# Performance work log

Measured on AMD Instinct MI355X. Metric: run time of the kernel, lower is better.

Reference implementation:

```python
import jax, jax.numpy as jnp
import numpy as np

EPS = 1e-15
B, N, F, K = 16, 1024, 512, 128  # graphs, max_nodes, feat dim, clusters


def setup_inputs() -> dict:
    key = jax.random.key(0)
    k0, k1, k2 = jax.random.split(key, 3)
    rng = np.random.default_rng(0)
    # Ragged graph sizes (between N/2 and N nodes per graph)
    counts = rng.integers(N // 2, N + 1, size=B)
    T = int(counts.sum())
    batch = np.repeat(np.arange(B), counts)
    starts = np.repeat(np.concatenate([[0], np.cumsum(counts)[:-1]]), counts)
    column = np.arange(T) - starts
    flat_index = batch * N + column  # as in _build_motifpool_dense_layout
    mask_flat = np.zeros(B * N, dtype=bool)
    mask_flat[flat_index] = True
    mask = mask_flat.reshape(B, N)
    x = jax.random.normal(k0, (T, F), dtype=jnp.float32)
    s = jax.random.normal(k1, (T, K), dtype=jnp.float32)
    a = jax.random.uniform(k2, (B, N, N), dtype=jnp.float32)
    m = jnp.asarray(mask)
    adj = (a + a.transpose(0, 2, 1)) * m[:, :, None] * m[:, None, :]
    return {
        'x': x,
        's': s,
        'adj': adj,
        'flat_index': jnp.asarray(flat_index, dtype=jnp.int32),
        'mask': m,
    }


def reference(x, s, adj, flat_index, mask):
    Bn, Nn = mask.shape
    Fd = x.shape[-1]
    Kd = s.shape[-1]
    # ragged -> dense scatter (index_copy_ equivalent)
    xd = jnp.zeros((Bn * Nn, Fd), x.dtype).at[flat_index].set(x).reshape(Bn, Nn, Fd)
    sd = jnp.zeros((Bn * Nn, Kd), s.dtype).at[flat_index].set(s).reshape(Bn, Nn, Kd)
    fmask = mask[..., None].astype(x.dtype)  # [B,N,1]
    sm = jax.nn.softmax(sd, axis=-1) * fmask
    xm = xd * fmask
    # pooled features and adjacency
    out = jnp.einsum('bnk,bnf->bkf', sm, xm)
    sa = jnp.einsum('bnk,bnm->bkm', sm, adj)
    out_adj = jnp.einsum('bkm,bml->bkl', sa, sm)
    # mincut loss: tr(S^T A S) / tr(S^T D S)
    mincut_num = jnp.trace(out_adj, axis1=-2, axis2=-1)
    d_flat = adj.sum(-1)  # node degrees [B,N]
    mincut_den = jnp.einsum('bn,bnk,bnk->b', d_flat, sm, sm)
    mincut_loss = jnp.mean(-(mincut_num / mincut_den))
    # orthogonality loss
    ss = jnp.einsum('bnk,bnl->bkl', sm, sm)
    ss_norm = jnp.linalg.norm(ss, axis=(-2, -1), keepdims=True)
    i_s = jnp.eye(Kd, dtype=ss.dtype)
    ortho_loss = jnp.mean(
        jnp.linalg.norm(ss / ss_norm - i_s / jnp.sqrt(jnp.asarray(Kd, ss.dtype)),
                        axis=(-2, -1)))
    # zero diagonal, symmetric degree-normalize
    eye_b = jnp.eye(Kd, dtype=bool)
    out_adj = jnp.where(eye_b, jnp.zeros((), out_adj.dtype), out_adj)
    d = jnp.sqrt(out_adj.sum(-1))[:, None, :] + EPS  # [B,1,K]
    out_adj = out_adj / d / d.transpose(0, 2, 1)
    return (sm, out, out_adj, mincut_loss, ortho_loss)
```

## Files before the change

kernel.cpp:

```cpp
#include <hip/hip_runtime.h>

constexpr int NB = 16, NN = 1024, NF = 512, NK = 128;
constexpr int NCH = 8;
constexpr int MSPLIT = 2;
constexpr float EPSV = 1e-15f;

__global__ __launch_bounds__(256) void k_build_rowof(const int* __restrict__ fidx,
                                                     int* __restrict__ rowof, int T) {
  int t = blockIdx.x * 256 + threadIdx.x;
  if (t < T) rowof[fidx[t]] = t;
}

__global__ __launch_bounds__(256) void k_softmax(const float* __restrict__ s,
                                                 const int* __restrict__ rowof,
                                                 float* __restrict__ sm) {
  int d = blockIdx.x * 4 + (threadIdx.x >> 6);
  int lane = threadIdx.x & 63;
  float* orow = sm + (size_t)d * NK;
  int ri = rowof[d];
  if (ri < 0) {
    orow[lane] = 0.f;
    orow[lane + 64] = 0.f;
    return;
  }
  const float* row = s + (size_t)ri * NK;
  float a = row[lane], b2 = row[lane + 64];
  float m = fmaxf(a, b2);
#pragma unroll
  for (int off = 32; off; off >>= 1) m = fmaxf(m, __shfl_xor(m, off, 64));
  float e0 = expf(a - m), e1 = expf(b2 - m);
  float ssum = e0 + e1;
#pragma unroll
  for (int off = 32; off; off >>= 1) ssum += __shfl_xor(ssum, off, 64);
  float inv = 1.0f / ssum;
  orow[lane] = e0 * inv;
  orow[lane + 64] = e1 * inv;
}

__global__ __launch_bounds__(256) void k_adj_sm(const float* __restrict__ adj,
                                                const float* __restrict__ sm,
                                                float* __restrict__ Yp,
                                                float* __restrict__ dfp) {
  __shared__ float At[64][68];
  __shared__ float Ss[64][128];
  int b = blockIdx.y;
  int n0 = blockIdx.x * 64;
  int z = blockIdx.z;
  const float* A = adj + (size_t)b * NN * NN;
  const float* S = sm + (size_t)b * NN * NK;
  int tid = threadIdx.x;
  int tr = tid >> 4, tc = tid & 15;
  int r0 = tr * 4, c0 = tc * 8;
  float acc[4][8] = {};
  float rsum[4] = {0.f, 0.f, 0.f, 0.f};
  for (int m0 = z * (NN / MSPLIT); m0 < (z + 1) * (NN / MSPLIT); m0 += 64) {
    __syncthreads();
#pragma unroll
    for (int p = 0; p < 4; ++p) {
      int r = p * 16 + tr;
      float4 v = *(const float4*)(A + (size_t)(n0 + r) * NN + m0 + tc * 4);
      *(float4*)&At[r][tc * 4] = v;
      float ps = v.x + v.y + v.z + v.w;
      ps += __shfl_xor(ps, 1, 64); ps += __shfl_xor(ps, 2, 64);
      ps += __shfl_xor(ps, 4, 64); ps += __shfl_xor(ps, 8, 64);
      rsum[p] += ps;
    }
#pragma unroll
    for (int p = 0; p < 8; ++p) {
      int r = p * 8 + (tid >> 5);
      int c = (tid & 31) * 4;
      *(float4*)&Ss[r][c] = *(const float4*)(S + (size_t)(m0 + r) * NK + c);
    }
    __syncthreads();
#pragma unroll
    for (int mm = 0; mm < 64; ++mm) {
      float a0 = At[r0 + 0][mm], a1 = At[r0 + 1][mm];
      float a2 = At[r0 + 2][mm], a3 = At[r0 + 3][mm];
      float bb[8];
      *(float4*)&bb[0] = *(const float4*)&Ss[mm][c0];
      *(float4*)&bb[4] = *(const float4*)&Ss[mm][c0 + 4];
#pragma unroll
      for (int j = 0; j < 8; ++j) {
        acc[0][j] = fmaf(a0, bb[j], acc[0][j]);
        acc[1][j] = fmaf(a1, bb[j], acc[1][j]);
        acc[2][j] = fmaf(a2, bb[j], acc[2][j]);
        acc[3][j] = fmaf(a3, bb[j], acc[3][j]);
      }
    }
  }
  float* Yb = Yp + ((size_t)z * NB + b) * NN * NK;
#pragma unroll
  for (int i = 0; i < 4; ++i) {
    *(float4*)(Yb + (size_t)(n0 + r0 + i) * NK + c0) = *(float4*)&acc[i][0];
    *(float4*)(Yb + (size_t)(n0 + r0 + i) * NK + c0 + 4) = *(float4*)&acc[i][4];
  }
  if (tc == 0) {
#pragma unroll
    for (int p = 0; p < 4; ++p)
      dfp[((size_t)z * NB + b) * NN + n0 + p * 16 + tr] = rsum[p];
  }
}

__global__ __launch_bounds__(256) void k_dflat(const float* __restrict__ dfp,
                                               float* __restrict__ dflat) {
  int i = blockIdx.x * 256 + threadIdx.x;
  dflat[i] = dfp[i] + dfp[NB * NN + i];
}

__global__ __launch_bounds__(512) void k_feat(const float* __restrict__ sm,
                                              const float* __restrict__ x,
                                              const int* __restrict__ rowof,
                                              float* __restrict__ out0,
                                              float* __restrict__ out1) {
  __shared__ float Ss[64][128];
  __shared__ float Xs[64][68];
  int b = blockIdx.y;
  int fbase = blockIdx.x * 64;
  int z = blockIdx.z;
  const float* S = sm + (size_t)b * NN * NK;
  int tid = threadIdx.x;
  int tk = tid >> 4, tf = tid & 15;
  int k0 = tk * 4, f0 = tf * 4;
  float acc[4][4] = {};
  for (int n0 = z * (NN / 2); n0 < (z + 1) * (NN / 2); n0 += 64) {
    __syncthreads();
#pragma unroll
    for (int p = 0; p < 4; ++p) {
      int r = p * 16 + (tid >> 5);
      int c = (tid & 31) * 4;
      *(float4*)&Ss[r][c] = *(const float4*)(S + (size_t)(n0 + r) * NK + c);
    }
#pragma unroll
    for (int p = 0; p < 2; ++p) {
      int r = p * 32 + (tid >> 4);
      int c = (tid & 15) * 4;
      int ri = rowof[b * NN + n0 + r];
      float4 v = make_float4(0.f, 0.f, 0.f, 0.f);
      if (ri >= 0) v = *(const float4*)(x + (size_t)ri * NF + fbase + c);
      *(float4*)&Xs[r][c] = v;
    }
    __syncthreads();
#pragma unroll
    for (int nn = 0; nn < 64; ++nn) {
      float a[4], bb[4];
      *(float4*)a = *(const float4*)&Ss[nn][k0];
      *(float4*)bb = *(const float4*)&Xs[nn][f0];
#pragma unroll
      for (int i = 0; i < 4; ++i)
#pragma unroll
        for (int j = 0; j < 4; ++j)
          acc[i][j] = fmaf(a[i], bb[j], acc[i][j]);
    }
  }
  float* O = (z ? out1 : out0) + (size_t)b * NK * NF;
#pragma unroll
  for (int i = 0; i < 4; ++i)
    *(float4*)(O + (size_t)(k0 + i) * NF + fbase + f0) = *(float4*)&acc[i][0];
}

__global__ __launch_bounds__(256) void k_red_feat(float* __restrict__ out0,
                                                  const float* __restrict__ out1) {
  size_t i = (size_t)blockIdx.x * 256 + threadIdx.x;
  float4 a = ((const float4*)out0)[i];
  float4 c = ((const float4*)out1)[i];
  a.x += c.x; a.y += c.y; a.z += c.z; a.w += c.w;
  ((float4*)out0)[i] = a;
}

__global__ __launch_bounds__(512) void k_tt(const float* __restrict__ sm,
                                            const float* __restrict__ Yp,
                                            const float* __restrict__ dflat,
                                            float* __restrict__ padj,
                                            float* __restrict__ pss,
                                            float* __restrict__ denb) {
  __shared__ float Ls[32][128];
  __shared__ float Rs[32][128];
  __shared__ float red[512];
  int ch = blockIdx.x, b = blockIdx.y, z = blockIdx.z;
  int nbase = ch * 128;
  const float* L = sm + (size_t)b * NN * NK;
  const float* R0 = Yp + (size_t)b * NN * NK;
  const float* R1 = Yp + ((size_t)NB + b) * NN * NK;
  float* O = (z ? pss : padj) + ((size_t)ch * NB + b) * NK * NK;
  int tid = threadIdx.x;
  int tkk = tid >> 5, tcc = tid & 31;
  int k0 = tkk * 8, c0 = tcc * 4;
  int lr = tid >> 4, c4 = tid & 15;
  float acc[8][4] = {};
  float denp = 0.f;
  float (&RR)[32][128] = z ? Ls : Rs;
  for (int n0 = 0; n0 < 128; n0 += 32) {
    __syncthreads();
    int grow = nbase + n0 + lr;
    const float* Lp = L + (size_t)grow * NK;
    float df = z ? dflat[b * NN + grow] : 0.f;
#pragma unroll
    for (int j = 0; j < 2; ++j) {
      int cc = (c4 + 16 * j) * 4;
      float4 v = *(const float4*)(Lp + cc);
      *(float4*)&Ls[lr][cc] = v;
      if (z) {
        denp += df * (v.x * v.x + v.y * v.y + v.z * v.z + v.w * v.w);
      } else {
        float4 r0v = *(const float4*)(R0 + (size_t)grow * NK + cc);
        float4 r1v = *(const float4*)(R1 + (size_t)grow * NK + cc);
        r0v.x += r1v.x; r0v.y += r1v.y; r0v.z += r1v.z; r0v.w += r1v.w;
        *(float4*)&Rs[lr][cc] = r0v;
      }
    }
    __syncthreads();
#pragma unroll
    for (int nn = 0; nn < 32; ++nn) {
      float a[8], bb[4];
      *(float4*)&a[0] = *(const float4*)&Ls[nn][k0];
      *(float4*)&a[4] = *(const float4*)&Ls[nn][k0 + 4];
      *(float4*)bb = *(const float4*)&RR[nn][c0];
#pragma unroll
      for (int i = 0; i < 8; ++i)
#pragma unroll
        for (int j = 0; j < 4; ++j)
          acc[i][j] = fmaf(a[i], bb[j], acc[i][j]);
    }
  }
#pragma unroll
  for (int i = 0; i < 8; ++i)
    *(float4*)&O[(size_t)(k0 + i) * NK + c0] = *(float4*)&acc[i][0];
  if (z) {
    red[tid] = denp;
    __syncthreads();
#pragma unroll
    for (int sft = 256; sft; sft >>= 1) {
      if (tid < sft) red[tid] += red[tid + sft];
      __syncthreads();
    }
    if (tid == 0) atomicAdd(&denb[b], red[0]);
  }
}

__global__ __launch_bounds__(256) void k_reduce(const float* __restrict__ padj,
                                                const float* __restrict__ pss,
                                                float* __restrict__ adjraw,
                                                float* __restrict__ ssb) {
  size_t i = (size_t)blockIdx.x * 256 + threadIdx.x;
  size_t stride4 = (size_t)NB * NK * NK / 4;
  const float4* pa = (const float4*)padj + i;
  const float4* ps = (const float4*)pss + i;
  float4 a = make_float4(0.f, 0.f, 0.f, 0.f);
  float4 s = make_float4(0.f, 0.f, 0.f, 0.f);
#pragma unroll
  for (int ch = 0; ch < NCH; ++ch) {
    float4 va = pa[(size_t)ch * stride4];
    float4 vs = ps[(size_t)ch * stride4];
    a.x += va.x; a.y += va.y; a.z += va.z; a.w += va.w;
    s.x += vs.x; s.y += vs.y; s.z += vs.z; s.w += vs.w;
  }
  ((float4*)adjraw)[i] = a;
  ((float4*)ssb)[i] = s;
}

__device__ __forceinline__ float block_reduce_sum(float v, float* red) {
  int tid = threadIdx.x;
  red[tid] = v;
  __syncthreads();
#pragma unroll
  for (int sft = 128; sft; sft >>= 1) {
    if (tid < sft) red[tid] += red[tid + sft];
    __syncthreads();
  }
  float r = red[0];
  __syncthreads();
  return r;
}

__global__ __launch_bounds__(256) void k_finalize(const float* __restrict__ denb,
                                                  const float* __restrict__ ssb,
                                                  float* __restrict__ out_adj,
                                                  float* __restrict__ out_loss) {
  __shared__ float red[256];
  __shared__ float sd[NK];
  int b = blockIdx.x, tid = threadIdx.x;
  float* AR = out_adj + (size_t)b * NK * NK;
  const float* SS = ssb + (size_t)b * NK * NK;

  float tv = (tid < NK) ? AR[tid * NK + tid] : 0.f;
  float trace = block_reduce_sum(tv, red);
  float den = denb[b];

  float n2 = 0.f;
  for (int i4 = tid; i4 < NK * NK / 4; i4 += 256) {
    float4 v = *(const float4*)(SS + (size_t)i4 * 4);
    n2 += v.x * v.x + v.y * v.y + v.z * v.z + v.w * v.w;
  }
  float nrm = sqrtf(block_reduce_sum(n2, red));

  const float isk = 0.08838834764831845f;
  float osum = 0.f;
  for (int i = tid; i < NK * NK; i += 256) {
    int r = i >> 7, c = i & (NK - 1);
    float val = SS[i] / nrm - ((r == c) ? isk : 0.f);
    osum += val * val;
  }
  float ortho = sqrtf(block_reduce_sum(osum, red));

  if (tid < NK) {
    float rsumv = 0.f;
    const float* row = AR + (size_t)tid * NK;
    for (int j = 0; j < NK; ++j) rsumv += (j == tid) ? 0.f : row[j];
    sd[tid] = sqrtf(rsumv) + EPSV;
  }
  __syncthreads();

  for (int i = tid; i < NK * NK; i += 256) {
    int r = i >> 7, c = i & (NK - 1);
    AR[i] = (r == c) ? 0.f : AR[i] / (sd[r] * sd[c]);
  }

  if (tid == 0) {
    atomicAdd(&out_loss[0], -(trace / den) * (1.0f / NB));
    atomicAdd(&out_loss[1], ortho * (1.0f / NB));
  }
}

extern "C" void kernel_launch(void* const* d_in, const int* in_sizes, int n_in,
                              void* d_out, int out_size, void* d_ws, size_t ws_size,
                              hipStream_t stream) {
  const float* x = (const float*)d_in[0];
  const float* s = (const float*)d_in[1];
  const float* adj = (const float*)d_in[2];
  const int* fidx = (const int*)d_in[3];
  int T = in_sizes[3];

  float* out_sm = (float*)d_out;
  float* out_feat = out_sm + (size_t)NB * NN * NK;
  float* out_adj = out_feat + (size_t)NB * NK * NF;
  float* out_loss = out_adj + (size_t)NB * NK * NK;

  float* Yp = (float*)d_ws;
  float* dfp = Yp + (size_t)MSPLIT * NB * NN * NK;
  float* dflat = dfp + (size_t)MSPLIT * NB * NN;
  float* padj = dflat + (size_t)NB * NN;
  float* pss = padj + (size_t)NCH * NB * NK * NK;
  float* ssb = pss + (size_t)NCH * NB * NK * NK;
  float* outf1 = ssb + (size_t)NB * NK * NK;
  float* denb = outf1 + (size_t)NB * NK * NF;
  int* rowof = (int*)(denb + NB);

  hipMemsetAsync(out_loss, 0, 2 * sizeof(float), stream);
  hipMemsetAsync(denb, 0, NB * sizeof(float), stream);
  hipMemsetAsync(rowof, 0xFF, (size_t)NB * NN * sizeof(int), stream);

  k_build_rowof<<<(T + 255) / 256, 256, 0, stream>>>(fidx, rowof, T);
  k_softmax<<<NB * NN / 4, 256, 0, stream>>>(s, rowof, out_sm);
  k_adj_sm<<<dim3(NN / 64, NB, MSPLIT), 256, 0, stream>>>(adj, out_sm, Yp, dfp);
  k_dflat<<<NB * NN / 256, 256, 0, stream>>>(dfp, dflat);
  k_feat<<<dim3(NF / 64, NB, 2), 512, 0, stream>>>(out_sm, x, rowof, out_feat, outf1);
  k_red_feat<<<NB * NK * NF / 4 / 256, 256, 0, stream>>>(out_feat, outf1);
  k_tt<<<dim3(NCH, NB, 2), 512, 0, stream>>>(out_sm, Yp, dflat, padj, pss, denb);
  k_reduce<<<NB * NK * NK / 4 / 256, 256, 0, stream>>>(padj, pss, out_adj, ssb);
  k_finalize<<<NB, 256, 0, stream>>>(denb, ssb, out_adj, out_loss);
}
```

Before: 285.2 us.

## Use split-bf16 MFMA for adjacency and pooled-product GEMMs with transposed softmax

Moves the adj×S and S^T×Y / S^T×S products from scalar FP32 FMA loops onto bf16 MFMA instructions. Operands are split into hi and lo bf16 parts and combined with three MFMAs per tile so accuracy stays close to FP32. The softmax kernel now also writes a transposed hi/lo bf16 copy of S, and Y is stored transposed so both GEMMs get K-contiguous operands. The aim is to cut the ALU-bound FP32 matmul time, at the cost of extra workspace traffic, more conversion work, and small precision loss from the three-term split.

```diff
diff --git a/kernel.cpp b/kernel.cpp
--- a/kernel.cpp
+++ b/kernel.cpp
@@ -5,6 +5,26 @@
 constexpr int MSPLIT = 2;
 constexpr float EPSV = 1e-15f;
 
+typedef __attribute__((ext_vector_type(8))) short bf16x8;
+typedef __attribute__((ext_vector_type(4))) float f32x4;
+
+__device__ __forceinline__ f32x4 MFMA(bf16x8 a, bf16x8 b, f32x4 c) {
+  return __builtin_amdgcn_mfma_f32_16x16x32_bf16(a, b, c, 0, 0, 0);
+}
+
+__device__ __forceinline__ unsigned short bf16_rn(float f) {
+  unsigned int u = __float_as_uint(f);
+  u += 0x7fffu + ((u >> 16) & 1u);
+  return (unsigned short)(u >> 16);
+}
+__device__ __forceinline__ float bf16f(unsigned short h) {
+  return __uint_as_float((unsigned int)h << 16);
+}
+__device__ __forceinline__ void split2(float f, unsigned short& h, unsigned short& lo) {
+  h = bf16_rn(f);
+  lo = bf16_rn(f - bf16f(h));
+}
+
 __global__ __launch_bounds__(256) void k_build_rowof(const int* __restrict__ fidx,
                                                      int* __restrict__ rowof, int T) {
   int t = blockIdx.x * 256 + threadIdx.x;
@@ -13,92 +33,137 @@
 
 __global__ __launch_bounds__(256) void k_softmax(const float* __restrict__ s,
                                                  const int* __restrict__ rowof,
-                                                 float* __restrict__ sm) {
-  int d = blockIdx.x * 4 + (threadIdx.x >> 6);
-  int lane = threadIdx.x & 63;
-  float* orow = sm + (size_t)d * NK;
-  int ri = rowof[d];
-  if (ri < 0) {
-    orow[lane] = 0.f;
-    orow[lane + 64] = 0.f;
-    return;
-  }
-  const float* row = s + (size_t)ri * NK;
-  float a = row[lane], b2 = row[lane + 64];
-  float m = fmaxf(a, b2);
-#pragma unroll
-  for (int off = 32; off; off >>= 1) m = fmaxf(m, __shfl_xor(m, off, 64));
-  float e0 = expf(a - m), e1 = expf(b2 - m);
-  float ssum = e0 + e1;
-#pragma unroll
-  for (int off = 32; off; off >>= 1) ssum += __shfl_xor(ssum, off, 64);
-  float inv = 1.0f / ssum;
-  orow[lane] = e0 * inv;
-  orow[lane + 64] = e1 * inv;
+                                                 float* __restrict__ sm,
+                                                 unsigned short* __restrict__ smTh,
+                                                 unsigned short* __restrict__ smTl) {
+  __shared__ float P[64][129];
+  int blk = blockIdx.x;
+  int b = blk >> 4, n0 = (blk & 15) * 64;
+  int tid = threadIdx.x, wv = tid >> 6, lane = tid & 63;
+  for (int i = 0; i < 16; ++i) {
+    int r = wv * 16 + i;
+    int ri = rowof[b * NN + n0 + r];
+    float e0 = 0.f, e1 = 0.f;
+    if (ri >= 0) {
+      const float* row = s + (size_t)ri * NK;
+      float a = row[lane], c = row[lane + 64];
+      float m = fmaxf(a, c);
+#pragma unroll
+      for (int off = 32; off; off >>= 1) m = fmaxf(m, __shfl_xor(m, off, 64));
+      e0 = expf(a - m);
+      e1 = expf(c - m);
+      float sum = e0 + e1;
+#pragma unroll
+      for (int off = 32; off; off >>= 1) sum += __shfl_xor(sum, off, 64);
+      float inv = 1.0f / sum;
+      e0 *= inv;
+      e1 *= inv;
+    }
+    P[r][lane] = e0;
+    P[r][lane + 64] = e1;
+  }
+  __syncthreads();
+  int r2 = tid >> 2, cb = (tid & 3) * 32;
+  float* orow = sm + ((size_t)b * NN + n0 + r2) * NK + cb;
+#pragma unroll
+  for (int j = 0; j < 8; ++j) {
+    float4 v = make_float4(P[r2][cb + j * 4], P[r2][cb + j * 4 + 1],
+                           P[r2][cb + j * 4 + 2], P[r2][cb + j * 4 + 3]);
+    *(float4*)(orow + j * 4) = v;
+  }
+  for (int j = 0; j < 32; ++j) {
+    int k = wv * 32 + j;
+    float v = P[lane][k];
+    unsigned short h, lo;
+    split2(v, h, lo);
+    size_t off = ((size_t)b * NK + k) * NN + n0 + lane;
+    smTh[off] = h;
+    smTl[off] = lo;
+  }
 }
 
 __global__ __launch_bounds__(256) void k_adj_sm(const float* __restrict__ adj,
-                                                const float* __restrict__ sm,
-                                                float* __restrict__ Yp,
+                                                const unsigned short* __restrict__ smTh,
+                                                const unsigned short* __restrict__ smTl,
+                                                float* __restrict__ Ytp,
                                                 float* __restrict__ dfp) {
-  __shared__ float At[64][68];
-  __shared__ float Ss[64][128];
-  int b = blockIdx.y;
-  int n0 = blockIdx.x * 64;
-  int z = blockIdx.z;
+  __shared__ __align__(16) unsigned short STh[128][72], STl[128][72];
+  __shared__ __align__(16) unsigned short ADh[64][72], ADl[64][72];
+  int b = blockIdx.y, n0 = blockIdx.x * 64, z = blockIdx.z;
+  int tid = threadIdx.x, wv = tid >> 6, l = tid & 63;
+  int lr = l & 15, lk = l >> 4;
+  int tk = tid >> 1, th = tid & 1;
+  int sn = tid >> 2, sq = tid & 3;
   const float* A = adj + (size_t)b * NN * NN;
-  const float* S = sm + (size_t)b * NN * NK;
-  int tid = threadIdx.x;
-  int tr = tid >> 4, tc = tid & 15;
-  int r0 = tr * 4, c0 = tc * 8;
-  float acc[4][8] = {};
-  float rsum[4] = {0.f, 0.f, 0.f, 0.f};
+  f32x4 zero = {0.f, 0.f, 0.f, 0.f};
+  f32x4 acc[2][4];
+#pragma unroll
+  for (int i = 0; i < 2; ++i)
+#pragma unroll
+    for (int j = 0; j < 4; ++j) acc[i][j] = zero;
+  float rsacc = 0.f;
   for (int m0 = z * (NN / MSPLIT); m0 < (z + 1) * (NN / MSPLIT); m0 += 64) {
     __syncthreads();
-#pragma unroll
-    for (int p = 0; p < 4; ++p) {
-      int r = p * 16 + tr;
-      float4 v = *(const float4*)(A + (size_t)(n0 + r) * NN + m0 + tc * 4);
-      *(float4*)&At[r][tc * 4] = v;
-      float ps = v.x + v.y + v.z + v.w;
-      ps += __shfl_xor(ps, 1, 64); ps += __shfl_xor(ps, 2, 64);
-      ps += __shfl_xor(ps, 4, 64); ps += __shfl_xor(ps, 8, 64);
-      rsum[p] += ps;
-    }
-#pragma unroll
-    for (int p = 0; p < 8; ++p) {
-      int r = p * 8 + (tid >> 5);
-      int c = (tid & 31) * 4;
-      *(float4*)&Ss[r][c] = *(const float4*)(S + (size_t)(m0 + r) * NK + c);
-    }
-    __syncthreads();
-#pragma unroll
-    for (int mm = 0; mm < 64; ++mm) {
-      float a0 = At[r0 + 0][mm], a1 = At[r0 + 1][mm];
-      float a2 = At[r0 + 2][mm], a3 = At[r0 + 3][mm];
-      float bb[8];
-      *(float4*)&bb[0] = *(const float4*)&Ss[mm][c0];
-      *(float4*)&bb[4] = *(const float4*)&Ss[mm][c0 + 4];
-#pragma unroll
-      for (int j = 0; j < 8; ++j) {
-        acc[0][j] = fmaf(a0, bb[j], acc[0][j]);
-        acc[1][j] = fmaf(a1, bb[j], acc[1][j]);
-        acc[2][j] = fmaf(a2, bb[j], acc[2][j]);
-        acc[3][j] = fmaf(a3, bb[j], acc[3][j]);
-      }
-    }
-  }
-  float* Yb = Yp + ((size_t)z * NB + b) * NN * NK;
-#pragma unroll
-  for (int i = 0; i < 4; ++i) {
-    *(float4*)(Yb + (size_t)(n0 + r0 + i) * NK + c0) = *(float4*)&acc[i][0];
-    *(float4*)(Yb + (size_t)(n0 + r0 + i) * NK + c0 + 4) = *(float4*)&acc[i][4];
-  }
-  if (tc == 0) {
-#pragma unroll
-    for (int p = 0; p < 4; ++p)
-      dfp[((size_t)z * NB + b) * NN + n0 + p * 16 + tr] = rsum[p];
-  }
+    {
+      const uint4* gh = (const uint4*)(smTh + ((size_t)b * NK + tk) * NN + m0 + th * 32);
+      const uint4* gl = (const uint4*)(smTl + ((size_t)b * NK + tk) * NN + m0 + th * 32);
+#pragma unroll
+      for (int j = 0; j < 4; ++j) {
+        *(uint4*)&STh[tk][th * 32 + j * 8] = gh[j];
+        *(uint4*)&STl[tk][th * 32 + j * 8] = gl[j];
+      }
+    }
+    {
+      const float* ap = A + (size_t)(n0 + sn) * NN + m0 + sq * 16;
+      float ps = 0.f;
+#pragma unroll
+      for (int j = 0; j < 4; ++j) {
+        float4 v = *(const float4*)(ap + j * 4);
+        ushort4 vh, vl;
+        split2(v.x, vh.x, vl.x);
+        split2(v.y, vh.y, vl.y);
+        split2(v.z, vh.z, vl.z);
+        split2(v.w, vh.w, vl.w);
+        *(ushort4*)&ADh[sn][sq * 16 + j * 4] = vh;
+        *(ushort4*)&ADl[sn][sq * 16 + j * 4] = vl;
+        ps += v.x + v.y + v.z + v.w;
+      }
+      ps += __shfl_xor(ps, 1, 64);
+      ps += __shfl_xor(ps, 2, 64);
+      rsacc += ps;
+    }
+    __syncthreads();
+#pragma unroll
+    for (int s = 0; s < 2; ++s) {
+      bf16x8 ah0 = *(const bf16x8*)&STh[wv * 32 + lr][s * 32 + lk * 8];
+      bf16x8 ah1 = *(const bf16x8*)&STh[wv * 32 + 16 + lr][s * 32 + lk * 8];
+      bf16x8 al0 = *(const bf16x8*)&STl[wv * 32 + lr][s * 32 + lk * 8];
+      bf16x8 al1 = *(const bf16x8*)&STl[wv * 32 + 16 + lr][s * 32 + lk * 8];
+#pragma unroll
+      for (int nt = 0; nt < 4; ++nt) {
+        bf16x8 bh = *(const bf16x8*)&ADh[nt * 16 + lr][s * 32 + lk * 8];
+        bf16x8 bl = *(const bf16x8*)&ADl[nt * 16 + lr][s * 32 + lk * 8];
+        acc[0][nt] = MFMA(ah0, bh, acc[0][nt]);
+        acc[0][nt] = MFMA(ah0, bl, acc[0][nt]);
+        acc[0][nt] = MFMA(al0, bh, acc[0][nt]);
+        acc[1][nt] = MFMA(ah1, bh, acc[1][nt]);
+        acc[1][nt] = MFMA(ah1, bl, acc[1][nt]);
+        acc[1][nt] = MFMA(al1, bh, acc[1][nt]);
+      }
+    }
+  }
+  float* Yb = Ytp + ((size_t)z * NB + b) * NK * NN;
+#pragma unroll
+  for (int kt = 0; kt < 2; ++kt)
+#pragma unroll
+    for (int nt = 0; nt < 4; ++nt)
+#pragma unroll
+      for (int reg = 0; reg < 4; ++reg) {
+        int k = wv * 32 + kt * 16 + lk * 4 + reg;
+        int n = n0 + nt * 16 + lr;
+        Yb[(size_t)k * NN + n] = acc[kt][nt][reg];
+      }
+  if (sq == 0) dfp[((size_t)z * NB + b) * NN + n0 + sn] = rsacc;
 }
 
 __global__ __launch_bounds__(256) void k_dflat(const float* __restrict__ dfp,
@@ -167,69 +232,98 @@
   ((float4*)out0)[i] = a;
 }
 
-__global__ __launch_bounds__(512) void k_tt(const float* __restrict__ sm,
-                                            const float* __restrict__ Yp,
+__global__ __launch_bounds__(256) void k_tt(const unsigned short* __restrict__ smTh,
+                                            const unsigned short* __restrict__ smTl,
+                                            const float* __restrict__ Ytp,
                                             const float* __restrict__ dflat,
                                             float* __restrict__ padj,
                                             float* __restrict__ pss,
                                             float* __restrict__ denb) {
-  __shared__ float Ls[32][128];
-  __shared__ float Rs[32][128];
-  __shared__ float red[512];
+  __shared__ __align__(16) unsigned short STh[128][40], STl[128][40];
+  __shared__ __align__(16) unsigned short YTh[128][40], YTl[128][40];
+  __shared__ float red[256];
   int ch = blockIdx.x, b = blockIdx.y, z = blockIdx.z;
   int nbase = ch * 128;
-  const float* L = sm + (size_t)b * NN * NK;
-  const float* R0 = Yp + (size_t)b * NN * NK;
-  const float* R1 = Yp + ((size_t)NB + b) * NN * NK;
+  int tid = threadIdx.x, wv = tid >> 6, l = tid & 63;
+  int lr = l & 15, lk = l >> 4;
+  int tk = tid >> 1, th = tid & 1;
+  f32x4 zero = {0.f, 0.f, 0.f, 0.f};
+  f32x4 acc[2][8];
+#pragma unroll
+  for (int i = 0; i < 2; ++i)
+#pragma unroll
+    for (int j = 0; j < 8; ++j) acc[i][j] = zero;
+  float denp = 0.f;
+  for (int c = 0; c < 4; ++c) {
+    int nn0 = nbase + c * 32;
+    __syncthreads();
+    {
+      const unsigned short* gh = smTh + ((size_t)b * NK + tk) * NN + nn0 + th * 16;
+      const unsigned short* gl = smTl + ((size_t)b * NK + tk) * NN + nn0 + th * 16;
+#pragma unroll
+      for (int j = 0; j < 4; ++j) {
+        ushort4 hj = *(const ushort4*)(gh + j * 4);
+        ushort4 lj = *(const ushort4*)(gl + j * 4);
+        *(ushort4*)&STh[tk][th * 16 + j * 4] = hj;
+        *(ushort4*)&STl[tk][th * 16 + j * 4] = lj;
+        if (z) {
+          float4 dv = *(const float4*)(dflat + (size_t)b * NN + nn0 + th * 16 + j * 4);
+          float v0 = bf16f(hj.x) + bf16f(lj.x), v1 = bf16f(hj.y) + bf16f(lj.y);
+          float v2 = bf16f(hj.z) + bf16f(lj.z), v3 = bf16f(hj.w) + bf16f(lj.w);
+          denp += dv.x * v0 * v0 + dv.y * v1 * v1 + dv.z * v2 * v2 + dv.w * v3 * v3;
+        }
+      }
+    }
+    if (!z) {
+      const float* y0 = Ytp + ((size_t)b * NK + tk) * NN + nn0 + th * 16;
+      const float* y1 = y0 + (size_t)NB * NK * NN;
+#pragma unroll
+      for (int j = 0; j < 4; ++j) {
+        float4 a = *(const float4*)(y0 + j * 4);
+        float4 cc = *(const float4*)(y1 + j * 4);
+        a.x += cc.x; a.y += cc.y; a.z += cc.z; a.w += cc.w;
+        ushort4 vh, vl;
+        split2(a.x, vh.x, vl.x);
+        split2(a.y, vh.y, vl.y);
+        split2(a.z, vh.z, vl.z);
+        split2(a.w, vh.w, vl.w);
+        *(ushort4*)&YTh[tk][th * 16 + j * 4] = vh;
+        *(ushort4*)&YTl[tk][th * 16 + j * 4] = vl;
+      }
+    }
+    __syncthreads();
+    unsigned short(*Bh)[40] = z ? STh : YTh;
+    unsigned short(*Bl)[40] = z ? STl : YTl;
+    bf16x8 ah0 = *(const bf16x8*)&STh[wv * 32 + lr][lk * 8];
+    bf16x8 ah1 = *(const bf16x8*)&STh[wv * 32 + 16 + lr][lk * 8];
+    bf16x8 al0 = *(const bf16x8*)&STl[wv * 32 + lr][lk * 8];
+    bf16x8 al1 = *(const bf16x8*)&STl[wv * 32 + 16 + lr][lk * 8];
+#pragma unroll
+    for (int ct = 0; ct < 8; ++ct) {
+      bf16x8 bh = *(const bf16x8*)&Bh[ct * 16 + lr][lk * 8];
+      bf16x8 bl = *(const bf16x8*)&Bl[ct * 16 + lr][lk * 8];
+      acc[0][ct] = MFMA(ah0, bh, acc[0][ct]);
+      acc[0][ct] = MFMA(ah0, bl, acc[0][ct]);
+      acc[0][ct] = MFMA(al0, bh, acc[0][ct]);
+      acc[1][ct] = MFMA(ah1, bh, acc[1][ct]);
+      acc[1][ct] = MFMA(ah1, bl, acc[1][ct]);
+      acc[1][ct] = MFMA(al1, bh, acc[1][ct]);
+    }
+  }
   float* O = (z ? pss : padj) + ((size_t)ch * NB + b) * NK * NK;
-  int tid = threadIdx.x;
-  int tkk = tid >> 5, tcc = tid & 31;
-  int k0 = tkk * 8, c0 = tcc * 4;
-  int lr = tid >> 4, c4 = tid & 15;
-  float acc[8][4] = {};
-  float denp = 0.f;
-  float (&RR)[32][128] = z ? Ls : Rs;
-  for (int n0 = 0; n0 < 128; n0 += 32) {
-    __syncthreads();
-    int grow = nbase + n0 + lr;
-    const float* Lp = L + (size_t)grow * NK;
-    float df = z ? dflat[b * NN + grow] : 0.f;
-#pragma unroll
-    for (int j = 0; j < 2; ++j) {
-      int cc = (c4 + 16 * j) * 4;
-      float4 v = *(const float4*)(Lp + cc);
-      *(float4*)&Ls[lr][cc] = v;
-      if (z) {
-        denp += df * (v.x * v.x + v.y * v.y + v.z * v.z + v.w * v.w);
-      } else {
-        float4 r0v = *(const float4*)(R0 + (size_t)grow * NK + cc);
-        float4 r1v = *(const float4*)(R1 + (size_t)grow * NK + cc);
-        r0v.x += r1v.x; r0v.y += r1v.y; r0v.z += r1v.z; r0v.w += r1v.w;
-        *(float4*)&Rs[lr][cc] = r0v;
-      }
-    }
-    __syncthreads();
-#pragma unroll
-    for (int nn = 0; nn < 32; ++nn) {
-      float a[8], bb[4];
-      *(float4*)&a[0] = *(const float4*)&Ls[nn][k0];
-      *(float4*)&a[4] = *(const float4*)&Ls[nn][k0 + 4];
-      *(float4*)bb = *(const float4*)&RR[nn][c0];
-#pragma unroll
-      for (int i = 0; i < 8; ++i)
-#pragma unroll
-        for (int j = 0; j < 4; ++j)
-          acc[i][j] = fmaf(a[i], bb[j], acc[i][j]);
-    }
-  }
-#pragma unroll
-  for (int i = 0; i < 8; ++i)
-    *(float4*)&O[(size_t)(k0 + i) * NK + c0] = *(float4*)&acc[i][0];
+#pragma unroll
+  for (int kt = 0; kt < 2; ++kt)
+#pragma unroll
+    for (int ct = 0; ct < 8; ++ct)
+#pragma unroll
+      for (int reg = 0; reg < 4; ++reg)
+        O[(size_t)(wv * 32 + kt * 16 + lk * 4 + reg) * NK + ct * 16 + lr] =
+            acc[kt][ct][reg];
   if (z) {
     red[tid] = denp;
     __syncthreads();
 #pragma unroll
-    for (int sft = 256; sft; sft >>= 1) {
+    for (int sft = 128; sft; sft >>= 1) {
       if (tid < sft) red[tid] += red[tid + sft];
       __syncthreads();
     }
@@ -335,27 +429,29 @@
   float* out_adj = out_feat + (size_t)NB * NK * NF;
   float* out_loss = out_adj + (size_t)NB * NK * NK;
 
-  float* Yp = (float*)d_ws;
-  float* dfp = Yp + (size_t)MSPLIT * NB * NN * NK;
-  float* dflat = dfp + (size_t)MSPLIT * NB * NN;
+  float* Ytp = (float*)d_ws;
+  float* dfp = Ytp + (size_t)2 * NB * NK * NN;
+  float* dflat = dfp + (size_t)2 * NB * NN;
   float* padj = dflat + (size_t)NB * NN;
   float* pss = padj + (size_t)NCH * NB * NK * NK;
   float* ssb = pss + (size_t)NCH * NB * NK * NK;
   float* outf1 = ssb + (size_t)NB * NK * NK;
   float* denb = outf1 + (size_t)NB * NK * NF;
-  int* rowof = (int*)(denb + NB);
+  unsigned short* smTh = (unsigned short*)(denb + 16);
+  unsigned short* smTl = smTh + (size_t)NB * NK * NN;
+  int* rowof = (int*)(smTl + (size_t)NB * NK * NN);
 
   hipMemsetAsync(out_loss, 0, 2 * sizeof(float), stream);
-  hipMemsetAsync(denb, 0, NB * sizeof(float), stream);
+  hipMemsetAsync(denb, 0, 16 * sizeof(float), stream);
   hipMemsetAsync(rowof, 0xFF, (size_t)NB * NN * sizeof(int), stream);
 
   k_build_rowof<<<(T + 255) / 256, 256, 0, stream>>>(fidx, rowof, T);
-  k_softmax<<<NB * NN / 4, 256, 0, stream>>>(s, rowof, out_sm);
-  k_adj_sm<<<dim3(NN / 64, NB, MSPLIT), 256, 0, stream>>>(adj, out_sm, Yp, dfp);
+  k_softmax<<<NB * NN / 64, 256, 0, stream>>>(s, rowof, out_sm, smTh, smTl);
+  k_adj_sm<<<dim3(NN / 64, NB, MSPLIT), 256, 0, stream>>>(adj, smTh, smTl, Ytp, dfp);
   k_dflat<<<NB * NN / 256, 256, 0, stream>>>(dfp, dflat);
   k_feat<<<dim3(NF / 64, NB, 2), 512, 0, stream>>>(out_sm, x, rowof, out_feat, outf1);
   k_red_feat<<<NB * NK * NF / 4 / 256, 256, 0, stream>>>(out_feat, outf1);
-  k_tt<<<dim3(NCH, NB, 2), 512, 0, stream>>>(out_sm, Yp, dflat, padj, pss, denb);
+  k_tt<<<dim3(NCH, NB, 2), 256, 0, stream>>>(smTh, smTl, Ytp, dflat, padj, pss, denb);
   k_reduce<<<NB * NK * NK / 4 / 256, 256, 0, stream>>>(padj, pss, out_adj, ssb);
   k_finalize<<<NB, 256, 0, stream>>>(denb, ssb, out_adj, out_loss);
 }
```

Result: faster. 279.6 us (-2.0%).
